# Kernel optimization log

Hardware: AMD Instinct MI355X
Metric: run time of the kernel (lower is better)

Reference implementation:

```python
import jax, jax.numpy as jnp
import numpy as np

N_SEQ, N_TOK, C_M, C, C_Z = 512, 384, 64, 32, 128


def setup_inputs() -> dict:
    key = jax.random.key(0)
    k1, k2, k3, k4 = jax.random.split(key, 4)
    scale = 1.0 / np.sqrt(C_M)
    return {
        "msa_feat": jax.random.normal(k1, (N_SEQ, N_TOK, C_M), dtype=jnp.float32),
        "msa_mask": jnp.ones((N_SEQ, N_TOK), dtype=jnp.float32),
        "gamma": jnp.ones((C_M,), dtype=jnp.float32),
        "beta": jnp.zeros((C_M,), dtype=jnp.float32),
        "Wa": jax.random.normal(k2, (C_M, C), dtype=jnp.float32) * scale,
        "Wb": jax.random.normal(k3, (C_M, C), dtype=jnp.float32) * scale,
        "Wout": jax.random.normal(k4, (C * C, C_Z), dtype=jnp.float32) * (1.0 / C),
        "bout": jnp.zeros((C_Z,), dtype=jnp.float32),
    }


def reference(msa_feat, msa_mask, gamma, beta, Wa, Wb, Wout, bout):
    # LayerNorm over c_m (eps matches torch default 1e-5)
    mu = jnp.mean(msa_feat, axis=-1, keepdims=True)
    var = jnp.mean(jnp.square(msa_feat - mu), axis=-1, keepdims=True)
    m = (msa_feat - mu) * jax.lax.rsqrt(var + 1e-5) * gamma + beta

    mask = msa_mask[..., None]                       # [s, i, 1]
    a = (m @ Wa) * mask                              # [s, i, c]
    b = (m @ Wb) * mask                              # [s, j, c]

    # Outer product contracted over MSA rows s: [i, j, c, c]
    ab = jnp.einsum('sic,sjd->ijcd', a, b)
    n_tok = a.shape[-2]
    ab = ab.reshape(n_tok, n_tok, C * C)             # [i, j, c*c]

    z = ab @ Wout + bout                             # [i, j, c_z]
    norm = jnp.einsum('si,sj->ij', msa_mask, msa_mask)
    return z / (norm[..., None] + 0.001)
```

## Files before the change

### kernel.cpp

```cpp
#include <hip/hip_runtime.h>
#include <cstdint>
#include <cstddef>

#define NS 512
#define NT 384
#define CZ 128

typedef __bf16 bf16x8 __attribute__((ext_vector_type(8)));
typedef __bf16 bf16x4 __attribute__((ext_vector_type(4)));
typedef float floatx16 __attribute__((ext_vector_type(16)));


__global__ __launch_bounds__(256) void prep_wout(const float* __restrict__ Wout,
                                                 __bf16* __restrict__ WT) {
  const int idx = blockIdx.x * 256 + threadIdx.x;
  const int e = idx >> 10, kk = idx & 1023;
  const int round = kk >> 9, rem = kk & 511, d = rem >> 4, cp = rem & 15;
  const int c = round * 16 + cp;
  WT[idx] = (__bf16)Wout[(size_t)(c * 32 + d) * CZ + e];
}

__global__ __launch_bounds__(256) void prep_norm(const float* __restrict__ mask,
                                                 float* __restrict__ rnorm) {
  __shared__ float mi[512];
  const int i = blockIdx.x, t = threadIdx.x;
  mi[t]       = mask[(size_t)t * NT + i];
  mi[t + 256] = mask[(size_t)(t + 256) * NT + i];
  __syncthreads();
  for (int j = t; j < NT; j += 256) {
    float acc = 0.f;
#pragma unroll 4
    for (int s = 0; s < NS; ++s) acc += mi[s] * mask[(size_t)s * NT + j];
    rnorm[(size_t)i * NT + j] = 1.0f / (acc + 0.001f);
  }
}

__global__ __launch_bounds__(64) void ln_proj(const float* __restrict__ feat,
                                              const float* __restrict__ mask,
                                              const float* __restrict__ gamma,
                                              const float* __restrict__ beta,
                                              const float* __restrict__ Wa,
                                              const float* __restrict__ Wb,
                                              __bf16* __restrict__ Abf,
                                              __bf16* __restrict__ Bbf) {
  __shared__ float tile[64][65];
  __shared__ __bf16 T[32 * 72];
  const int bid = blockIdx.x;
  const int i = bid >> 3;
  const int s0 = (bid & 7) << 6;
  const int lane = threadIdx.x;
  const int l31 = lane & 31, lh = lane >> 5;

  const int rsub = lane >> 4, cb = (lane & 15) * 4;
#pragma unroll
  for (int rr = 0; rr < 16; ++rr) {
    const int row = rr * 4 + rsub;
    const float4 v = *(const float4*)(feat + ((size_t)(s0 + row) * NT + i) * 64 + cb);
    tile[row][cb] = v.x; tile[row][cb + 1] = v.y;
    tile[row][cb + 2] = v.z; tile[row][cb + 3] = v.w;
  }
  __syncthreads();

  float x[64];
#pragma unroll
  for (int k = 0; k < 64; ++k) x[k] = tile[lane][k];

  float mu = 0.f;
#pragma unroll
  for (int k = 0; k < 64; ++k) mu += x[k];
  mu *= (1.0f / 64.0f);
  float var = 0.f;
#pragma unroll
  for (int k = 0; k < 64; ++k) { const float d = x[k] - mu; var += d * d; }
  var *= (1.0f / 64.0f);
  const float rstd = rsqrtf(var + 1e-5f);
#pragma unroll
  for (int k = 0; k < 64; ++k)
    x[k] = (x[k] - mu) * rstd * gamma[k] + beta[k];

  const float mv = mask[(size_t)(s0 + lane) * NT + i];

  float acc[32];
#pragma unroll
  for (int c = 0; c < 32; ++c) acc[c] = 0.f;
#pragma unroll 8
  for (int k = 0; k < 64; ++k) {
    const float mk = x[k];
#pragma unroll
    for (int c = 0; c < 32; ++c) acc[c] = fmaf(mk, Wa[k * 32 + c], acc[c]);
  }
#pragma unroll
  for (int c = 0; c < 32; ++c) T[c * 72 + lane] = (__bf16)(acc[c] * mv);
  __syncthreads();
  {
    __bf16* dst = Abf + (size_t)(i >> 2) * 65536 + (size_t)(s0 >> 3) * 1024 +
                  (size_t)((i & 3) * 32) * 8;
#pragma unroll
    for (int q = 0; q < 4; ++q) {
      const bf16x8 v = *(const bf16x8*)(T + l31 * 72 + (q * 2 + lh) * 8);
      *(bf16x8*)(dst + (size_t)(q * 2 + lh) * 1024 + l31 * 8) = v;
    }
  }
  __syncthreads();

#pragma unroll
  for (int c = 0; c < 32; ++c) acc[c] = 0.f;
#pragma unroll 8
  for (int k = 0; k < 64; ++k) {
    const float mk = x[k];
#pragma unroll
    for (int c = 0; c < 32; ++c) acc[c] = fmaf(mk, Wb[k * 32 + c], acc[c]);
  }
#pragma unroll
  for (int c = 0; c < 32; ++c) T[c * 72 + lane] = (__bf16)(acc[c] * mv);
  __syncthreads();
  {
    __bf16* dst = Bbf + (size_t)(i >> 3) * 131072 + (size_t)(s0 >> 3) * 2048 +
                  (size_t)((i & 7) * 32) * 8;
#pragma unroll
    for (int q = 0; q < 4; ++q) {
      const bf16x8 v = *(const bf16x8*)(T + l31 * 72 + (q * 2 + lh) * 8);
      *(bf16x8*)(dst + (size_t)(q * 2 + lh) * 2048 + l31 * 8) = v;
    }
  }
}

__global__ __launch_bounds__(256) void opm_gemm(const __bf16* __restrict__ A,
                                                const __bf16* __restrict__ B,
                                                const __bf16* __restrict__ WT,
                                                const float* __restrict__ bout,
                                                const float* __restrict__ rnorm,
                                                float* __restrict__ out) {
  __shared__ __align__(16) __bf16 smem[24576];

  const int t = threadIdx.x, lane = t & 63, wid = t >> 6;
  const int wm = wid & 1, wn = wid >> 1;
  const int l31 = lane & 31, lh = lane >> 5;
  const int bm = blockIdx.x % 96, bn = blockIdx.x / 96;

  const __bf16* Apan = A + (size_t)bm * 65536;
  const __bf16* Bpan = B + (size_t)bn * 131072;

  floatx16 acc[2][4];
#pragma unroll
  for (int fm = 0; fm < 2; ++fm)
#pragma unroll
    for (int fn = 0; fn < 4; ++fn)
#pragma unroll
      for (int q = 0; q < 16; ++q) acc[fm][fn][q] = 0.f;

#define STAGE(kt, buf)                                                          \
  {                                                                             \
    __bf16* dst = smem + (buf) * 12288;                                         \
    _Pragma("unroll")                                                           \
    for (int g2 = 0; g2 < 2; ++g2) {                                            \
      const int g = wid * 2 + g2;                                               \
      __builtin_amdgcn_global_load_lds(                                         \
          (const __attribute__((address_space(1))) void*)(Apan + (kt) * 4096 +  \
                                                          g * 512 + lane * 8),  \
          (__attribute__((address_space(3))) void*)(dst + g * 512), 16, 0, 0);  \
    }                                                                           \
    _Pragma("unroll")                                                           \
    for (int g4 = 0; g4 < 4; ++g4) {                                            \
      const int g = wid * 4 + g4;                                               \
      __builtin_amdgcn_global_load_lds(                                         \
          (const __attribute__((address_space(1))) void*)(Bpan + (kt) * 8192 +  \
                                                          g * 512 + lane * 8),  \
          (__attribute__((address_space(3))) void*)(dst + 4096 + g * 512),      \
          16, 0, 0);                                                            \
    }                                                                           \
  }

  STAGE(0, 0);
  int buf = 0;
  for (int kt = 0; kt < 16; ++kt) {
    __syncthreads();
    if (kt < 15) STAGE(kt + 1, buf ^ 1);
    const __bf16* As = smem + buf * 12288;
    const __bf16* Bs = As + 4096;
#pragma unroll
    for (int ks = 0; ks < 2; ++ks) {
      const int ck = ks * 2 + lh;
      bf16x8 af[2], bf[4];
#pragma unroll
      for (int fm = 0; fm < 2; ++fm)
        af[fm] = *(const bf16x8*)(As + ck * 1024 + (wm * 64 + fm * 32 + l31) * 8);
#pragma unroll
      for (int fn = 0; fn < 4; ++fn)
        bf[fn] = *(const bf16x8*)(Bs + ck * 2048 + (wn * 128 + fn * 32 + l31) * 8);
#pragma unroll
      for (int fm = 0; fm < 2; ++fm)
#pragma unroll
        for (int fn = 0; fn < 4; ++fn)
          acc[fm][fn] = __builtin_amdgcn_mfma_f32_32x32x16_bf16(af[fm], bf[fn],
                                                                acc[fm][fn], 0, 0, 0);
    }
    buf ^= 1;
  }
#undef STAGE

  floatx16 z;
#pragma unroll
  for (int q = 0; q < 16; ++q) z[q] = 0.f;
  const int e = wid * 32 + l31;

#pragma unroll
  for (int round = 0; round < 2; ++round) {
    __syncthreads();
#pragma unroll
    for (int fm = 0; fm < 2; ++fm)
#pragma unroll
      for (int fn = 0; fn < 4; ++fn) {
        const int p = (wm * 2 + fm) * 8 + wn * 4 + fn;
        __bf16* base = smem + p * 648 + l31 * 20 + lh * 4;
#pragma unroll
        for (int qp = 0; qp < 2; ++qp) {
          bf16x4 v;
#pragma unroll
          for (int j = 0; j < 4; ++j)
            v[j] = (__bf16)acc[fm][fn][round * 8 + qp * 4 + j];
          *(bf16x4*)(base + qp * 8) = v;
        }
      }
    __syncthreads();
    const __bf16* wrow = WT + (size_t)e * 1024 + round * 512 + lh * 8;
    const __bf16* prow = smem + l31 * 648 + lh * 8;
#pragma unroll 8
    for (int ks = 0; ks < 32; ++ks) {
      const bf16x8 pa = *(const bf16x8*)(prow + ks * 20);
      const bf16x8 wb = *(const bf16x8*)(wrow + ks * 16);
      z = __builtin_amdgcn_mfma_f32_32x32x16_bf16(pa, wb, z, 0, 0, 0);
    }
  }

  const float be = bout[e];
#pragma unroll
  for (int r = 0; r < 16; ++r) {
    const int p = (r & 3) + 8 * (r >> 2) + 4 * lh;
    const int i = bm * 4 + (p >> 3), j = bn * 8 + (p & 7);
    const float rn = rnorm[(size_t)i * NT + j];
    out[((size_t)i * NT + j) * CZ + e] = (z[r] + be) * rn;
  }
}

extern "C" void kernel_launch(void* const* d_in, const int* in_sizes, int n_in,
                              void* d_out, int out_size, void* d_ws, size_t ws_size,
                              hipStream_t stream) {
  const float* feat  = (const float*)d_in[0];
  const float* mask  = (const float*)d_in[1];
  const float* gamma = (const float*)d_in[2];
  const float* beta  = (const float*)d_in[3];
  const float* Wa    = (const float*)d_in[4];
  const float* Wb    = (const float*)d_in[5];
  const float* Wout  = (const float*)d_in[6];
  const float* bout  = (const float*)d_in[7];
  float* out = (float*)d_out;

  char* ws = (char*)d_ws;
  const size_t AB_BYTES = (size_t)96 * 65536 * sizeof(__bf16);
  __bf16* Abf = (__bf16*)(ws);
  __bf16* Bbf = (__bf16*)(ws + AB_BYTES);
  __bf16* WT  = (__bf16*)(ws + 2 * AB_BYTES);
  float* rnorm = (float*)(ws + 2 * AB_BYTES + (size_t)CZ * 1024 * sizeof(__bf16));

  prep_wout<<<512, 256, 0, stream>>>(Wout, WT);
  prep_norm<<<NT, 256, 0, stream>>>(mask, rnorm);
  ln_proj<<<NT * (NS / 64), 64, 0, stream>>>(feat, mask, gamma, beta, Wa, Wb, Abf, Bbf);
  opm_gemm<<<96 * 48, 256, 0, stream>>>(Abf, Bbf, WT, bout, rnorm, out);
}
```

Baseline: 460.3 us.

## Load GEMM operands directly into registers, drop LDS staging, swizzle blocks

The outer-product GEMM now loads A and B fragments straight from global memory into double-buffered registers instead of staging them through LDS with global_load_lds, which removes the per-iteration barriers. Shared memory shrinks to only the epilogue buffer, launch bounds request two blocks per SM, and the block index is remapped into 4x4 tiles for better L2 reuse of A/B panels. The prep_wout transpose is rewritten to read coalesced and scatter writes. It raises register pressure from the fragment double-buffering and gives up LDS sharing of the tiles between waves, so each wave re-fetches from global or cache.

New measurement: 480.7 us. 4.4% more time.

```diff
diff --git a/kernel.cpp b/kernel.cpp
--- a/kernel.cpp
+++ b/kernel.cpp
@@ -14,10 +14,10 @@
 __global__ __launch_bounds__(256) void prep_wout(const float* __restrict__ Wout,
                                                  __bf16* __restrict__ WT) {
   const int idx = blockIdx.x * 256 + threadIdx.x;
-  const int e = idx >> 10, kk = idx & 1023;
-  const int round = kk >> 9, rem = kk & 511, d = rem >> 4, cp = rem & 15;
-  const int c = round * 16 + cp;
-  WT[idx] = (__bf16)Wout[(size_t)(c * 32 + d) * CZ + e];
+  const int cd = idx >> 7, e = idx & 127;
+  const int c = cd >> 5, d = cd & 31;
+  const int kk = (c >> 4) * 512 + d * 16 + (c & 15);
+  WT[(size_t)e * 1024 + kk] = (__bf16)Wout[idx];
 }
 
 __global__ __launch_bounds__(256) void prep_norm(const float* __restrict__ mask,
@@ -125,21 +125,24 @@
   }
 }
 
-__global__ __launch_bounds__(256) void opm_gemm(const __bf16* __restrict__ A,
-                                                const __bf16* __restrict__ B,
-                                                const __bf16* __restrict__ WT,
-                                                const float* __restrict__ bout,
-                                                const float* __restrict__ rnorm,
-                                                float* __restrict__ out) {
-  __shared__ __align__(16) __bf16 smem[24576];
+__global__ __launch_bounds__(256, 2) void opm_gemm(const __bf16* __restrict__ A,
+                                                   const __bf16* __restrict__ B,
+                                                   const __bf16* __restrict__ WT,
+                                                   const float* __restrict__ bout,
+                                                   const float* __restrict__ rnorm,
+                                                   float* __restrict__ out) {
+  __shared__ __align__(16) __bf16 smem[20736];
 
   const int t = threadIdx.x, lane = t & 63, wid = t >> 6;
   const int wm = wid & 1, wn = wid >> 1;
   const int l31 = lane & 31, lh = lane >> 5;
-  const int bm = blockIdx.x % 96, bn = blockIdx.x / 96;
-
-  const __bf16* Apan = A + (size_t)bm * 65536;
-  const __bf16* Bpan = B + (size_t)bn * 131072;
+
+  const int sq = blockIdx.x >> 4, r4 = blockIdx.x & 15;
+  const int bm = (sq % 24) * 4 + (r4 & 3);
+  const int bn = (sq / 24) * 4 + (r4 >> 2);
+
+  const __bf16* pA = A + (size_t)bm * 65536 + (size_t)lh * 1024 + (wm * 64 + l31) * 8;
+  const __bf16* pB = B + (size_t)bn * 131072 + (size_t)lh * 2048 + (wn * 128 + l31) * 8;
 
   floatx16 acc[2][4];
 #pragma unroll
@@ -149,55 +152,38 @@
 #pragma unroll
       for (int q = 0; q < 16; ++q) acc[fm][fn][q] = 0.f;
 
-#define STAGE(kt, buf)                                                          \
-  {                                                                             \
-    __bf16* dst = smem + (buf) * 12288;                                         \
-    _Pragma("unroll")                                                           \
-    for (int g2 = 0; g2 < 2; ++g2) {                                            \
-      const int g = wid * 2 + g2;                                               \
-      __builtin_amdgcn_global_load_lds(                                         \
-          (const __attribute__((address_space(1))) void*)(Apan + (kt) * 4096 +  \
-                                                          g * 512 + lane * 8),  \
-          (__attribute__((address_space(3))) void*)(dst + g * 512), 16, 0, 0);  \
-    }                                                                           \
-    _Pragma("unroll")                                                           \
-    for (int g4 = 0; g4 < 4; ++g4) {                                            \
-      const int g = wid * 4 + g4;                                               \
-      __builtin_amdgcn_global_load_lds(                                         \
-          (const __attribute__((address_space(1))) void*)(Bpan + (kt) * 8192 +  \
-                                                          g * 512 + lane * 8),  \
-          (__attribute__((address_space(3))) void*)(dst + 4096 + g * 512),      \
-          16, 0, 0);                                                            \
-    }                                                                           \
-  }
-
-  STAGE(0, 0);
-  int buf = 0;
+  bf16x8 fa[2][2][2], fb[2][2][4];
+
+#define LOADKT(kt, b)                                                         \
+  {                                                                           \
+    _Pragma("unroll")                                                         \
+    for (int ks = 0; ks < 2; ++ks) {                                          \
+      _Pragma("unroll")                                                       \
+      for (int fm = 0; fm < 2; ++fm)                                          \
+        fa[b][ks][fm] =                                                       \
+            *(const bf16x8*)(pA + (kt) * 4096 + ks * 2048 + fm * 256);        \
+      _Pragma("unroll")                                                       \
+      for (int fn = 0; fn < 4; ++fn)                                          \
+        fb[b][ks][fn] =                                                       \
+            *(const bf16x8*)(pB + (kt) * 8192 + ks * 4096 + fn * 256);        \
+    }                                                                         \
+  }
+
+  LOADKT(0, 0);
+#pragma unroll 2
   for (int kt = 0; kt < 16; ++kt) {
-    __syncthreads();
-    if (kt < 15) STAGE(kt + 1, buf ^ 1);
-    const __bf16* As = smem + buf * 12288;
-    const __bf16* Bs = As + 4096;
-#pragma unroll
-    for (int ks = 0; ks < 2; ++ks) {
-      const int ck = ks * 2 + lh;
-      bf16x8 af[2], bf[4];
+    const int b = kt & 1;
+    if (kt < 15) LOADKT(kt + 1, b ^ 1);
+#pragma unroll
+    for (int ks = 0; ks < 2; ++ks)
 #pragma unroll
       for (int fm = 0; fm < 2; ++fm)
-        af[fm] = *(const bf16x8*)(As + ck * 1024 + (wm * 64 + fm * 32 + l31) * 8);
-#pragma unroll
-      for (int fn = 0; fn < 4; ++fn)
-        bf[fn] = *(const bf16x8*)(Bs + ck * 2048 + (wn * 128 + fn * 32 + l31) * 8);
-#pragma unroll
-      for (int fm = 0; fm < 2; ++fm)
 #pragma unroll
         for (int fn = 0; fn < 4; ++fn)
-          acc[fm][fn] = __builtin_amdgcn_mfma_f32_32x32x16_bf16(af[fm], bf[fn],
-                                                                acc[fm][fn], 0, 0, 0);
-    }
-    buf ^= 1;
-  }
-#undef STAGE
+          acc[fm][fn] = __builtin_amdgcn_mfma_f32_32x32x16_bf16(
+              fa[b][ks][fm], fb[b][ks][fn], acc[fm][fn], 0, 0, 0);
+  }
+#undef LOADKT
 
   floatx16 z;
 #pragma unroll
@@ -206,7 +192,6 @@
 
 #pragma unroll
   for (int round = 0; round < 2; ++round) {
-    __syncthreads();
 #pragma unroll
     for (int fm = 0; fm < 2; ++fm)
 #pragma unroll
@@ -231,6 +216,7 @@
       const bf16x8 wb = *(const bf16x8*)(wrow + ks * 16);
       z = __builtin_amdgcn_mfma_f32_32x32x16_bf16(pa, wb, z, 0, 0, 0);
     }
+    if (round == 0) __syncthreads();
   }
 
   const float be = bout[e];
```

## Shrink GEMM B-tile to 6 tokens, swizzle block order, batch norm kernel

Applied to the files above, without the earlier changes.

The outer-product GEMM tile shrinks from 4x8 to 4x6 token pairs. B is relaid out into 64 panels of 6 tokens, LDS per block drops, and launch bounds request 3 blocks per CU to raise occupancy and give 6144 blocks. Blocks are remapped in 4x4 groups to improve L2 reuse of A and B panels. The mask-norm kernel now computes 16 rows per block with register accumulators instead of one row per block, which cuts redundant mask reads. The trade-off is less reuse per tile and an epilogue that uses only 24 of the 32 MFMA output rows.

Result: slower. 513.3 us (+11.5%).

```diff
diff --git a/kernel.cpp b/kernel.cpp
--- a/kernel.cpp
+++ b/kernel.cpp
@@ -15,24 +15,40 @@
                                                  __bf16* __restrict__ WT) {
   const int idx = blockIdx.x * 256 + threadIdx.x;
   const int e = idx >> 10, kk = idx & 1023;
-  const int round = kk >> 9, rem = kk & 511, d = rem >> 4, cp = rem & 15;
-  const int c = round * 16 + cp;
+  const int c = ((kk >> 9) << 4) | (kk & 15);
+  const int d = (kk >> 4) & 31;
   WT[idx] = (__bf16)Wout[(size_t)(c * 32 + d) * CZ + e];
 }
 
-__global__ __launch_bounds__(256) void prep_norm(const float* __restrict__ mask,
+__global__ __launch_bounds__(384) void prep_norm(const float* __restrict__ mask,
                                                  float* __restrict__ rnorm) {
-  __shared__ float mi[512];
-  const int i = blockIdx.x, t = threadIdx.x;
-  mi[t]       = mask[(size_t)t * NT + i];
-  mi[t + 256] = mask[(size_t)(t + 256) * NT + i];
-  __syncthreads();
-  for (int j = t; j < NT; j += 256) {
-    float acc = 0.f;
-#pragma unroll 4
-    for (int s = 0; s < NS; ++s) acc += mi[s] * mask[(size_t)s * NT + j];
-    rnorm[(size_t)i * NT + j] = 1.0f / (acc + 0.001f);
-  }
+  __shared__ float mi[16][512];
+  const int i0 = blockIdx.x * 16, t = threadIdx.x;
+  for (int idx = t; idx < 16 * 512; idx += 384) {
+    const int ii = idx >> 9, s = idx & 511;
+    mi[ii][s] = mask[(size_t)s * NT + i0 + ii];
+  }
+  __syncthreads();
+  const int j = t;
+  float acc[16];
+#pragma unroll
+  for (int ii = 0; ii < 16; ++ii) acc[ii] = 0.f;
+  for (int s4 = 0; s4 < NS; s4 += 4) {
+    float mj[4];
+#pragma unroll
+    for (int q = 0; q < 4; ++q) mj[q] = mask[(size_t)(s4 + q) * NT + j];
+#pragma unroll
+    for (int ii = 0; ii < 16; ++ii) {
+      const float4 m4 = *(const float4*)&mi[ii][s4];
+      acc[ii] = fmaf(m4.x, mj[0], acc[ii]);
+      acc[ii] = fmaf(m4.y, mj[1], acc[ii]);
+      acc[ii] = fmaf(m4.z, mj[2], acc[ii]);
+      acc[ii] = fmaf(m4.w, mj[3], acc[ii]);
+    }
+  }
+#pragma unroll
+  for (int ii = 0; ii < 16; ++ii)
+    rnorm[(size_t)(i0 + ii) * NT + j] = 1.0f / (acc[ii] + 0.001f);
 }
 
 __global__ __launch_bounds__(64) void ln_proj(const float* __restrict__ feat,
@@ -115,43 +131,47 @@
   for (int c = 0; c < 32; ++c) T[c * 72 + lane] = (__bf16)(acc[c] * mv);
   __syncthreads();
   {
-    __bf16* dst = Bbf + (size_t)(i >> 3) * 131072 + (size_t)(s0 >> 3) * 2048 +
-                  (size_t)((i & 7) * 32) * 8;
+    const int pb = i / 6, jl = i % 6;
+    __bf16* dst = Bbf + (size_t)pb * 98304 + (size_t)(s0 >> 3) * 1536 +
+                  (size_t)(jl * 32) * 8;
 #pragma unroll
     for (int q = 0; q < 4; ++q) {
       const bf16x8 v = *(const bf16x8*)(T + l31 * 72 + (q * 2 + lh) * 8);
-      *(bf16x8*)(dst + (size_t)(q * 2 + lh) * 2048 + l31 * 8) = v;
-    }
-  }
-}
-
-__global__ __launch_bounds__(256) void opm_gemm(const __bf16* __restrict__ A,
-                                                const __bf16* __restrict__ B,
-                                                const __bf16* __restrict__ WT,
-                                                const float* __restrict__ bout,
-                                                const float* __restrict__ rnorm,
-                                                float* __restrict__ out) {
-  __shared__ __align__(16) __bf16 smem[24576];
+      *(bf16x8*)(dst + (size_t)(q * 2 + lh) * 1536 + l31 * 8) = v;
+    }
+  }
+}
+
+__global__ __launch_bounds__(256, 3) void opm_gemm(const __bf16* __restrict__ A,
+                                                   const __bf16* __restrict__ B,
+                                                   const __bf16* __restrict__ WT,
+                                                   const float* __restrict__ bout,
+                                                   const float* __restrict__ rnorm,
+                                                   float* __restrict__ out) {
+  __shared__ __align__(16) __bf16 smem[20736];
 
   const int t = threadIdx.x, lane = t & 63, wid = t >> 6;
   const int wm = wid & 1, wn = wid >> 1;
   const int l31 = lane & 31, lh = lane >> 5;
-  const int bm = blockIdx.x % 96, bn = blockIdx.x / 96;
+
+  const int sq = blockIdx.x >> 4, r4 = blockIdx.x & 15;
+  const int bm = (sq % 24) * 4 + (r4 & 3);
+  const int bn = (sq / 24) * 4 + (r4 >> 2);
 
   const __bf16* Apan = A + (size_t)bm * 65536;
-  const __bf16* Bpan = B + (size_t)bn * 131072;
-
-  floatx16 acc[2][4];
+  const __bf16* Bpan = B + (size_t)bn * 98304;
+
+  floatx16 acc[2][3];
 #pragma unroll
   for (int fm = 0; fm < 2; ++fm)
 #pragma unroll
-    for (int fn = 0; fn < 4; ++fn)
+    for (int fn = 0; fn < 3; ++fn)
 #pragma unroll
       for (int q = 0; q < 16; ++q) acc[fm][fn][q] = 0.f;
 
 #define STAGE(kt, buf)                                                          \
   {                                                                             \
-    __bf16* dst = smem + (buf) * 12288;                                         \
+    __bf16* dst = smem + (buf) * 10240;                                         \
     _Pragma("unroll")                                                           \
     for (int g2 = 0; g2 < 2; ++g2) {                                            \
       const int g = wid * 2 + g2;                                               \
@@ -161,10 +181,10 @@
           (__attribute__((address_space(3))) void*)(dst + g * 512), 16, 0, 0);  \
     }                                                                           \
     _Pragma("unroll")                                                           \
-    for (int g4 = 0; g4 < 4; ++g4) {                                            \
-      const int g = wid * 4 + g4;                                               \
+    for (int g3 = 0; g3 < 3; ++g3) {                                            \
+      const int g = wid * 3 + g3;                                               \
       __builtin_amdgcn_global_load_lds(                                         \
-          (const __attribute__((address_space(1))) void*)(Bpan + (kt) * 8192 +  \
+          (const __attribute__((address_space(1))) void*)(Bpan + (kt) * 6144 +  \
                                                           g * 512 + lane * 8),  \
           (__attribute__((address_space(3))) void*)(dst + 4096 + g * 512),      \
           16, 0, 0);                                                            \
@@ -176,22 +196,22 @@
   for (int kt = 0; kt < 16; ++kt) {
     __syncthreads();
     if (kt < 15) STAGE(kt + 1, buf ^ 1);
-    const __bf16* As = smem + buf * 12288;
+    const __bf16* As = smem + buf * 10240;
     const __bf16* Bs = As + 4096;
 #pragma unroll
     for (int ks = 0; ks < 2; ++ks) {
       const int ck = ks * 2 + lh;
-      bf16x8 af[2], bf[4];
+      bf16x8 af[2], bf[3];
 #pragma unroll
       for (int fm = 0; fm < 2; ++fm)
         af[fm] = *(const bf16x8*)(As + ck * 1024 + (wm * 64 + fm * 32 + l31) * 8);
 #pragma unroll
-      for (int fn = 0; fn < 4; ++fn)
-        bf[fn] = *(const bf16x8*)(Bs + ck * 2048 + (wn * 128 + fn * 32 + l31) * 8);
+      for (int fn = 0; fn < 3; ++fn)
+        bf[fn] = *(const bf16x8*)(Bs + ck * 1536 + (wn * 96 + fn * 32 + l31) * 8);
 #pragma unroll
       for (int fm = 0; fm < 2; ++fm)
 #pragma unroll
-        for (int fn = 0; fn < 4; ++fn)
+        for (int fn = 0; fn < 3; ++fn)
           acc[fm][fn] = __builtin_amdgcn_mfma_f32_32x32x16_bf16(af[fm], bf[fn],
                                                                 acc[fm][fn], 0, 0, 0);
     }
@@ -210,8 +230,8 @@
 #pragma unroll
     for (int fm = 0; fm < 2; ++fm)
 #pragma unroll
-      for (int fn = 0; fn < 4; ++fn) {
-        const int p = (wm * 2 + fm) * 8 + wn * 4 + fn;
+      for (int fn = 0; fn < 3; ++fn) {
+        const int p = (wm * 2 + fm) * 6 + wn * 3 + fn;
         __bf16* base = smem + p * 648 + l31 * 20 + lh * 4;
 #pragma unroll
         for (int qp = 0; qp < 2; ++qp) {
@@ -235,9 +255,9 @@
 
   const float be = bout[e];
 #pragma unroll
-  for (int r = 0; r < 16; ++r) {
+  for (int r = 0; r < 12; ++r) {
     const int p = (r & 3) + 8 * (r >> 2) + 4 * lh;
-    const int i = bm * 4 + (p >> 3), j = bn * 8 + (p & 7);
+    const int i = bm * 4 + p / 6, j = bn * 6 + p % 6;
     const float rn = rnorm[(size_t)i * NT + j];
     out[((size_t)i * NT + j) * CZ + e] = (z[r] + be) * rn;
   }
@@ -257,14 +277,15 @@
   float* out = (float*)d_out;
 
   char* ws = (char*)d_ws;
-  const size_t AB_BYTES = (size_t)96 * 65536 * sizeof(__bf16);
+  const size_t A_BYTES = (size_t)96 * 65536 * sizeof(__bf16);
+  const size_t B_BYTES = (size_t)64 * 98304 * sizeof(__bf16);
   __bf16* Abf = (__bf16*)(ws);
-  __bf16* Bbf = (__bf16*)(ws + AB_BYTES);
-  __bf16* WT  = (__bf16*)(ws + 2 * AB_BYTES);
-  float* rnorm = (float*)(ws + 2 * AB_BYTES + (size_t)CZ * 1024 * sizeof(__bf16));
+  __bf16* Bbf = (__bf16*)(ws + A_BYTES);
+  __bf16* WT  = (__bf16*)(ws + A_BYTES + B_BYTES);
+  float* rnorm = (float*)(ws + A_BYTES + B_BYTES + (size_t)CZ * 1024 * sizeof(__bf16));
 
   prep_wout<<<512, 256, 0, stream>>>(Wout, WT);
-  prep_norm<<<NT, 256, 0, stream>>>(mask, rnorm);
+  prep_norm<<<24, 384, 0, stream>>>(mask, rnorm);
   ln_proj<<<NT * (NS / 64), 64, 0, stream>>>(feat, mask, gamma, beta, Wa, Wb, Abf, Bbf);
-  opm_gemm<<<96 * 48, 256, 0, stream>>>(Abf, Bbf, WT, bout, rnorm, out);
-}
+  opm_gemm<<<96 * 64, 256, 0, stream>>>(Abf, Bbf, WT, bout, rnorm, out);
+}
```
